# Performance work log

Hardware: AMD Instinct MI355X
Metric: run time of the kernel (lower is better)

The kernel has to match this reference:

```python
import jax, jax.numpy as jnp
import numpy as np

N = 1_000_000   # half-edges
C = 64          # in_channels == out_channels (out = empty_like(x))


def setup_inputs() -> dict:
    key = jax.random.key(0)
    k1, k2, k3, k4, k5, k6 = jax.random.split(key, 6)
    x = jax.random.normal(k1, (N, C), dtype=jnp.float32)
    next_idx = jax.random.randint(k2, (N,), 0, N, dtype=jnp.int32)
    twin_idx = jax.random.randint(k3, (N,), 0, N, dtype=jnp.int32)
    has_twin = jax.random.randint(k4, (N,), 0, 2, dtype=jnp.int32).astype(jnp.bool_)
    # nn.Linear(2C, C): weight [C, 2C], bias [C]; kaiming-uniform-ish init scale
    bound = 1.0 / np.sqrt(2 * C)
    W = jax.random.uniform(k5, (C, 2 * C), dtype=jnp.float32, minval=-bound, maxval=bound)
    b = jax.random.uniform(k6, (C,), dtype=jnp.float32, minval=-bound, maxval=bound)
    return {"x": x, "next_idx": next_idx, "twin_idx": twin_idx,
            "has_twin": has_twin, "W": W, "b": b}


def reference(x, next_idx, twin_idx, has_twin, W, b):
    # per-half-edge gather of next/twin vertex features (twin zero-filled if absent)
    next_f = x[next_idx]                                   # [N, C]
    twin_f = jnp.where(has_twin[:, None], x[twin_idx], 0.0)  # [N, C]
    neighbor = jnp.concatenate([next_f, twin_f], axis=-1)  # [N, 2C]
    out = neighbor @ W.T + b                               # [N, C]
    return jax.nn.relu(out)
```

## Files before the change

### kernel.cpp

```cpp
#include <hip/hip_runtime.h>
#include <hip/hip_bf16.h>
#include <stdint.h>

typedef __attribute__((ext_vector_type(4))) float f32x4;
typedef __attribute__((ext_vector_type(8))) __bf16 bf16x8;

#define NROWS 1000000

__device__ __forceinline__ bf16x8 cvt8(f32x4 a, f32x4 b) {
    bf16x8 r;
    r[0] = (__bf16)a[0]; r[1] = (__bf16)a[1];
    r[2] = (__bf16)a[2]; r[3] = (__bf16)a[3];
    r[4] = (__bf16)b[0]; r[5] = (__bf16)b[1];
    r[6] = (__bf16)b[2]; r[7] = (__bf16)b[3];
    return r;
}

__global__ void heconv_mfma(const float* __restrict__ x,
                            const int* __restrict__ nidx,
                            const int* __restrict__ tidx,
                            const int* __restrict__ ht,
                            const float* __restrict__ W,
                            const float* __restrict__ bias,
                            float* __restrict__ out)
{
    const int lane = threadIdx.x & 63;
    const int wave = threadIdx.x >> 6;
    const int lrow = lane & 15;
    const int lkg  = lane >> 4;

    bf16x8 wfrag[4][4];
#pragma unroll
    for (int ct = 0; ct < 4; ++ct) {
        const float* wrow = W + (ct * 16 + lrow) * 128 + lkg * 8;
#pragma unroll
        for (int ks = 0; ks < 4; ++ks) {
            f32x4 w0 = *(const f32x4*)(wrow + ks * 32);
            f32x4 w1 = *(const f32x4*)(wrow + ks * 32 + 4);
            wfrag[ct][ks] = cvt8(w0, w1);
        }
    }
    f32x4 bfrag[4];
#pragma unroll
    for (int ct = 0; ct < 4; ++ct)
        bfrag[ct] = *(const f32x4*)(bias + ct * 16 + lkg * 4);

    const int nGroups = NROWS / 16;
    const int gstride = gridDim.x * 4;
    const int g0 = blockIdx.x * 4 + wave;

    int ni = 0, ti = 0, htv = 0;
    if (g0 < nGroups) {
        int r = g0 * 16 + lrow;
        ni = nidx[r]; ti = tidx[r]; htv = ht[r];
    }

    const f32x4 z = {0.f, 0.f, 0.f, 0.f};

    for (int g = g0; g < nGroups; g += gstride) {
        const float* pn = x + (size_t)ni * 64 + lkg * 8;
        f32x4 n0 = *(const f32x4*)(pn);
        f32x4 n1 = *(const f32x4*)(pn + 4);
        f32x4 n2 = *(const f32x4*)(pn + 32);
        f32x4 n3 = *(const f32x4*)(pn + 36);

        f32x4 t0 = z, t1 = z, t2 = z, t3 = z;
        if (htv) {
            const float* pt = x + (size_t)ti * 64 + lkg * 8;
            t0 = *(const f32x4*)(pt);
            t1 = *(const f32x4*)(pt + 4);
            t2 = *(const f32x4*)(pt + 32);
            t3 = *(const f32x4*)(pt + 36);
        }

        const int gn = g + gstride;
        int ni2 = 0, ti2 = 0, htv2 = 0;
        if (gn < nGroups) {
            int r = gn * 16 + lrow;
            ni2 = nidx[r]; ti2 = tidx[r]; htv2 = ht[r];
        }

        bf16x8 xf[4] = { cvt8(n0, n1), cvt8(n2, n3),
                         cvt8(t0, t1), cvt8(t2, t3) };
        const int r = g * 16 + lrow;
#pragma unroll
        for (int ct = 0; ct < 4; ++ct) {
            f32x4 acc = bfrag[ct];
#pragma unroll
            for (int ks = 0; ks < 4; ++ks)
                acc = __builtin_amdgcn_mfma_f32_16x16x32_bf16(wfrag[ct][ks], xf[ks], acc, 0, 0, 0);
            f32x4 o;
            o[0] = fmaxf(acc[0], 0.f);
            o[1] = fmaxf(acc[1], 0.f);
            o[2] = fmaxf(acc[2], 0.f);
            o[3] = fmaxf(acc[3], 0.f);
            *(f32x4*)(out + (size_t)r * 64 + ct * 16 + lkg * 4) = o;
        }

        ni = ni2; ti = ti2; htv = htv2;
    }
}

extern "C" void kernel_launch(void* const* d_in, const int* in_sizes, int n_in,
                              void* d_out, int out_size, void* d_ws, size_t ws_size,
                              hipStream_t stream) {
    const float* x    = (const float*)d_in[0];
    const int*   ni   = (const int*)d_in[1];
    const int*   ti   = (const int*)d_in[2];
    const int*   ht   = (const int*)d_in[3];
    const float* W    = (const float*)d_in[4];
    const float* bias = (const float*)d_in[5];
    float*       out  = (float*)d_out;

    heconv_mfma<<<2048, 256, 0, stream>>>(x, ni, ti, ht, W, bias, out);
}
```

Baseline: 156.8 us.

## Software-pipeline row gathers one iteration ahead and stage W fragments in LDS

The gathered x rows for the next group are now loaded before the current group's MFMAs run, and indices are prefetched two groups ahead, so gather latency overlaps compute. Weight fragments move from registers into shared memory, read per MFMA, and launch bounds of 256 threads with 4 blocks per CU are added. The aim is lower register pressure and higher occupancy plus latency hiding, at the cost of LDS reads in the inner loop and more live registers for the prefetched rows. The first-group load now runs without a bounds check.

Result: slower. 219.8 us (+40.2%).

```diff
diff --git a/kernel.cpp b/kernel.cpp
--- a/kernel.cpp
+++ b/kernel.cpp
@@ -16,79 +16,109 @@
     return r;
 }
 
-__global__ void heconv_mfma(const float* __restrict__ x,
-                            const int* __restrict__ nidx,
-                            const int* __restrict__ tidx,
-                            const int* __restrict__ ht,
-                            const float* __restrict__ W,
-                            const float* __restrict__ bias,
-                            float* __restrict__ out)
+__global__ __launch_bounds__(256, 4)
+void heconv_mfma(const float* __restrict__ x,
+                 const int* __restrict__ nidx,
+                 const int* __restrict__ tidx,
+                 const int* __restrict__ ht,
+                 const float* __restrict__ W,
+                 const float* __restrict__ bias,
+                 float* __restrict__ out)
 {
-    const int lane = threadIdx.x & 63;
-    const int wave = threadIdx.x >> 6;
+    __shared__ bf16x8 wlds[4][4][64];
+
+    const int tid  = threadIdx.x;
+    const int lane = tid & 63;
+    const int wave = tid >> 6;
     const int lrow = lane & 15;
     const int lkg  = lane >> 4;
 
-    bf16x8 wfrag[4][4];
-#pragma unroll
-    for (int ct = 0; ct < 4; ++ct) {
-        const float* wrow = W + (ct * 16 + lrow) * 128 + lkg * 8;
-#pragma unroll
-        for (int ks = 0; ks < 4; ++ks) {
-            f32x4 w0 = *(const f32x4*)(wrow + ks * 32);
-            f32x4 w1 = *(const f32x4*)(wrow + ks * 32 + 4);
-            wfrag[ct][ks] = cvt8(w0, w1);
-        }
+    for (int e = tid; e < 1024; e += 256) {
+        const int l  = e & 63;
+        const int ks = (e >> 6) & 3;
+        const int ct = e >> 8;
+        const float* wr = W + (ct * 16 + (l & 15)) * 128 + ks * 32 + (l >> 4) * 8;
+        f32x4 w0 = *(const f32x4*)(wr);
+        f32x4 w1 = *(const f32x4*)(wr + 4);
+        wlds[ct][ks][l] = cvt8(w0, w1);
     }
     f32x4 bfrag[4];
 #pragma unroll
     for (int ct = 0; ct < 4; ++ct)
         bfrag[ct] = *(const f32x4*)(bias + ct * 16 + lkg * 4);
+    __syncthreads();
 
     const int nGroups = NROWS / 16;
     const int gstride = gridDim.x * 4;
     const int g0 = blockIdx.x * 4 + wave;
 
-    int ni = 0, ti = 0, htv = 0;
-    if (g0 < nGroups) {
-        int r = g0 * 16 + lrow;
-        ni = nidx[r]; ti = tidx[r]; htv = ht[r];
-    }
-
     const f32x4 z = {0.f, 0.f, 0.f, 0.f};
 
-    for (int g = g0; g < nGroups; g += gstride) {
+    f32x4 n0, n1, n2, n3, t0, t1, t2, t3;
+    {
+        const int r = g0 * 16 + lrow;
+        const int ni = nidx[r];
+        const int tv = tidx[r];
+        const int hv = ht[r];
         const float* pn = x + (size_t)ni * 64 + lkg * 8;
-        f32x4 n0 = *(const f32x4*)(pn);
-        f32x4 n1 = *(const f32x4*)(pn + 4);
-        f32x4 n2 = *(const f32x4*)(pn + 32);
-        f32x4 n3 = *(const f32x4*)(pn + 36);
-
-        f32x4 t0 = z, t1 = z, t2 = z, t3 = z;
-        if (htv) {
-            const float* pt = x + (size_t)ti * 64 + lkg * 8;
+        n0 = *(const f32x4*)(pn);
+        n1 = *(const f32x4*)(pn + 4);
+        n2 = *(const f32x4*)(pn + 32);
+        n3 = *(const f32x4*)(pn + 36);
+        t0 = z; t1 = z; t2 = z; t3 = z;
+        if (hv) {
+            const float* pt = x + (size_t)tv * 64 + lkg * 8;
             t0 = *(const f32x4*)(pt);
             t1 = *(const f32x4*)(pt + 4);
             t2 = *(const f32x4*)(pt + 32);
             t3 = *(const f32x4*)(pt + 36);
         }
+    }
+    int niN = 0, tiN = 0, hvN = 0;
+    if (g0 + gstride < nGroups) {
+        const int r = (g0 + gstride) * 16 + lrow;
+        niN = nidx[r]; tiN = tidx[r]; hvN = ht[r];
+    }
 
-        const int gn = g + gstride;
-        int ni2 = 0, ti2 = 0, htv2 = 0;
-        if (gn < nGroups) {
-            int r = gn * 16 + lrow;
-            ni2 = nidx[r]; ti2 = tidx[r]; htv2 = ht[r];
+    for (int g = g0; g < nGroups; g += gstride) {
+        const int gN = g + gstride;
+
+        bf16x8 xf0 = cvt8(n0, n1);
+        bf16x8 xf1 = cvt8(n2, n3);
+        bf16x8 xf2 = cvt8(t0, t1);
+        bf16x8 xf3 = cvt8(t2, t3);
+
+        if (gN < nGroups) {
+            const float* pn = x + (size_t)niN * 64 + lkg * 8;
+            n0 = *(const f32x4*)(pn);
+            n1 = *(const f32x4*)(pn + 4);
+            n2 = *(const f32x4*)(pn + 32);
+            n3 = *(const f32x4*)(pn + 36);
+            t0 = z; t1 = z; t2 = z; t3 = z;
+            if (hvN) {
+                const float* pt = x + (size_t)tiN * 64 + lkg * 8;
+                t0 = *(const f32x4*)(pt);
+                t1 = *(const f32x4*)(pt + 4);
+                t2 = *(const f32x4*)(pt + 32);
+                t3 = *(const f32x4*)(pt + 36);
+            }
         }
 
-        bf16x8 xf[4] = { cvt8(n0, n1), cvt8(n2, n3),
-                         cvt8(t0, t1), cvt8(t2, t3) };
+        int ni2 = 0, ti2 = 0, hv2 = 0;
+        const int g2 = g + 2 * gstride;
+        if (g2 < nGroups) {
+            const int r = g2 * 16 + lrow;
+            ni2 = nidx[r]; ti2 = tidx[r]; hv2 = ht[r];
+        }
+
         const int r = g * 16 + lrow;
+        bf16x8 xf[4] = { xf0, xf1, xf2, xf3 };
 #pragma unroll
         for (int ct = 0; ct < 4; ++ct) {
             f32x4 acc = bfrag[ct];
 #pragma unroll
             for (int ks = 0; ks < 4; ++ks)
-                acc = __builtin_amdgcn_mfma_f32_16x16x32_bf16(wfrag[ct][ks], xf[ks], acc, 0, 0, 0);
+                acc = __builtin_amdgcn_mfma_f32_16x16x32_bf16(wlds[ct][ks][lane], xf[ks], acc, 0, 0, 0);
             f32x4 o;
             o[0] = fmaxf(acc[0], 0.f);
             o[1] = fmaxf(acc[1], 0.f);
@@ -97,7 +127,7 @@
             *(f32x4*)(out + (size_t)r * 64 + ct * 16 + lkg * 4) = o;
         }
 
-        ni = ni2; ti = ti2; htv = htv2;
+        niN = ni2; tiN = ti2; hvN = hv2;
     }
 }
 
```

## Double-buffer gathered features in registers and shrink grid to persistent waves

Applied to the files above, without the earlier changes.

Restructures the grid-stride loop into two interleaved stages (A/B). Each stage keeps its gathered x rows in registers one iteration ahead, with indices prefetched two iterations ahead. This lets the scattered loads overlap with the MFMA work. The grid is reduced to 512 blocks with launch bounds and sched_barriers to fix the instruction order. The trade-off is fewer resident waves, and therefore less latency hiding from occupancy, plus higher register pressure.

New measurement: 137.3 us, median of 2. 12.4% less time.

```diff
diff --git a/kernel.cpp b/kernel.cpp
--- a/kernel.cpp
+++ b/kernel.cpp
@@ -16,13 +16,14 @@
     return r;
 }
 
-__global__ void heconv_mfma(const float* __restrict__ x,
-                            const int* __restrict__ nidx,
-                            const int* __restrict__ tidx,
-                            const int* __restrict__ ht,
-                            const float* __restrict__ W,
-                            const float* __restrict__ bias,
-                            float* __restrict__ out)
+__global__ __launch_bounds__(256, 2)
+void heconv_mfma(const float* __restrict__ x,
+                 const int* __restrict__ nidx,
+                 const int* __restrict__ tidx,
+                 const int* __restrict__ ht,
+                 const float* __restrict__ W,
+                 const float* __restrict__ bias,
+                 float* __restrict__ out)
 {
     const int lane = threadIdx.x & 63;
     const int wave = threadIdx.x >> 6;
@@ -46,58 +47,162 @@
         bfrag[ct] = *(const f32x4*)(bias + ct * 16 + lkg * 4);
 
     const int nGroups = NROWS / 16;
-    const int gstride = gridDim.x * 4;
+    const int S  = gridDim.x * 4;
     const int g0 = blockIdx.x * 4 + wave;
 
-    int ni = 0, ti = 0, htv = 0;
-    if (g0 < nGroups) {
-        int r = g0 * 16 + lrow;
-        ni = nidx[r]; ti = tidx[r]; htv = ht[r];
-    }
-
     const f32x4 z = {0.f, 0.f, 0.f, 0.f};
 
-    for (int g = g0; g < nGroups; g += gstride) {
+    f32x4 pAn0, pAn1, pAn2, pAn3, pAt0, pAt1, pAt2, pAt3;
+    f32x4 pBn0, pBn1, pBn2, pBn3, pBt0, pBt1, pBt2, pBt3;
+
+    {
+        const int r = g0 * 16 + lrow;
+        const int ni = nidx[r], tv = tidx[r], hv = ht[r];
         const float* pn = x + (size_t)ni * 64 + lkg * 8;
-        f32x4 n0 = *(const f32x4*)(pn);
-        f32x4 n1 = *(const f32x4*)(pn + 4);
-        f32x4 n2 = *(const f32x4*)(pn + 32);
-        f32x4 n3 = *(const f32x4*)(pn + 36);
-
-        f32x4 t0 = z, t1 = z, t2 = z, t3 = z;
-        if (htv) {
-            const float* pt = x + (size_t)ti * 64 + lkg * 8;
-            t0 = *(const f32x4*)(pt);
-            t1 = *(const f32x4*)(pt + 4);
-            t2 = *(const f32x4*)(pt + 32);
-            t3 = *(const f32x4*)(pt + 36);
-        }
-
-        const int gn = g + gstride;
-        int ni2 = 0, ti2 = 0, htv2 = 0;
-        if (gn < nGroups) {
-            int r = gn * 16 + lrow;
-            ni2 = nidx[r]; ti2 = tidx[r]; htv2 = ht[r];
-        }
-
-        bf16x8 xf[4] = { cvt8(n0, n1), cvt8(n2, n3),
-                         cvt8(t0, t1), cvt8(t2, t3) };
-        const int r = g * 16 + lrow;
-#pragma unroll
-        for (int ct = 0; ct < 4; ++ct) {
-            f32x4 acc = bfrag[ct];
-#pragma unroll
-            for (int ks = 0; ks < 4; ++ks)
-                acc = __builtin_amdgcn_mfma_f32_16x16x32_bf16(wfrag[ct][ks], xf[ks], acc, 0, 0, 0);
-            f32x4 o;
-            o[0] = fmaxf(acc[0], 0.f);
-            o[1] = fmaxf(acc[1], 0.f);
-            o[2] = fmaxf(acc[2], 0.f);
-            o[3] = fmaxf(acc[3], 0.f);
-            *(f32x4*)(out + (size_t)r * 64 + ct * 16 + lkg * 4) = o;
-        }
-
-        ni = ni2; ti = ti2; htv = htv2;
+        pAn0 = *(const f32x4*)(pn);
+        pAn1 = *(const f32x4*)(pn + 4);
+        pAn2 = *(const f32x4*)(pn + 32);
+        pAn3 = *(const f32x4*)(pn + 36);
+        pAt0 = z; pAt1 = z; pAt2 = z; pAt3 = z;
+        if (hv) {
+            const float* pt = x + (size_t)tv * 64 + lkg * 8;
+            pAt0 = *(const f32x4*)(pt);
+            pAt1 = *(const f32x4*)(pt + 4);
+            pAt2 = *(const f32x4*)(pt + 32);
+            pAt3 = *(const f32x4*)(pt + 36);
+        }
+    }
+    pBn0 = z; pBn1 = z; pBn2 = z; pBn3 = z;
+    pBt0 = z; pBt1 = z; pBt2 = z; pBt3 = z;
+    if (g0 + S < nGroups) {
+        const int r = (g0 + S) * 16 + lrow;
+        const int ni = nidx[r], tv = tidx[r], hv = ht[r];
+        const float* pn = x + (size_t)ni * 64 + lkg * 8;
+        pBn0 = *(const f32x4*)(pn);
+        pBn1 = *(const f32x4*)(pn + 4);
+        pBn2 = *(const f32x4*)(pn + 32);
+        pBn3 = *(const f32x4*)(pn + 36);
+        if (hv) {
+            const float* pt = x + (size_t)tv * 64 + lkg * 8;
+            pBt0 = *(const f32x4*)(pt);
+            pBt1 = *(const f32x4*)(pt + 4);
+            pBt2 = *(const f32x4*)(pt + 32);
+            pBt3 = *(const f32x4*)(pt + 36);
+        }
+    }
+
+    int aNi = 0, aTi = 0, aHv = 0, bNi = 0, bTi = 0, bHv = 0;
+    if (g0 + 2 * S < nGroups) {
+        const int r = (g0 + 2 * S) * 16 + lrow;
+        aNi = nidx[r]; aTi = tidx[r]; aHv = ht[r];
+    }
+    if (g0 + 3 * S < nGroups) {
+        const int r = (g0 + 3 * S) * 16 + lrow;
+        bNi = nidx[r]; bTi = tidx[r]; bHv = ht[r];
+    }
+
+    for (int g = g0; g < nGroups; g += 2 * S) {
+        {
+            bf16x8 xf0 = cvt8(pAn0, pAn1);
+            bf16x8 xf1 = cvt8(pAn2, pAn3);
+            bf16x8 xf2 = cvt8(pAt0, pAt1);
+            bf16x8 xf3 = cvt8(pAt2, pAt3);
+
+            __builtin_amdgcn_sched_barrier(0);
+
+            if (g + 2 * S < nGroups) {
+                const float* pn = x + (size_t)aNi * 64 + lkg * 8;
+                pAn0 = *(const f32x4*)(pn);
+                pAn1 = *(const f32x4*)(pn + 4);
+                pAn2 = *(const f32x4*)(pn + 32);
+                pAn3 = *(const f32x4*)(pn + 36);
+                pAt0 = z; pAt1 = z; pAt2 = z; pAt3 = z;
+                if (aHv) {
+                    const float* pt = x + (size_t)aTi * 64 + lkg * 8;
+                    pAt0 = *(const f32x4*)(pt);
+                    pAt1 = *(const f32x4*)(pt + 4);
+                    pAt2 = *(const f32x4*)(pt + 32);
+                    pAt3 = *(const f32x4*)(pt + 36);
+                }
+            }
+
+            __builtin_amdgcn_sched_barrier(0);
+
+            aNi = 0; aTi = 0; aHv = 0;
+            if (g + 4 * S < nGroups) {
+                const int r = (g + 4 * S) * 16 + lrow;
+                aNi = nidx[r]; aTi = tidx[r]; aHv = ht[r];
+            }
+
+            const int r = g * 16 + lrow;
+            bf16x8 xf[4] = { xf0, xf1, xf2, xf3 };
+#pragma unroll
+            for (int ct = 0; ct < 4; ++ct) {
+                f32x4 acc = bfrag[ct];
+#pragma unroll
+                for (int ks = 0; ks < 4; ++ks)
+                    acc = __builtin_amdgcn_mfma_f32_16x16x32_bf16(wfrag[ct][ks], xf[ks], acc, 0, 0, 0);
+                f32x4 o;
+                o[0] = fmaxf(acc[0], 0.f);
+                o[1] = fmaxf(acc[1], 0.f);
+                o[2] = fmaxf(acc[2], 0.f);
+                o[3] = fmaxf(acc[3], 0.f);
+                *(f32x4*)(out + (size_t)r * 64 + ct * 16 + lkg * 4) = o;
+            }
+
+            __builtin_amdgcn_sched_barrier(0);
+        }
+
+        if (g + S < nGroups) {
+            bf16x8 xf0 = cvt8(pBn0, pBn1);
+            bf16x8 xf1 = cvt8(pBn2, pBn3);
+            bf16x8 xf2 = cvt8(pBt0, pBt1);
+            bf16x8 xf3 = cvt8(pBt2, pBt3);
+
+            __builtin_amdgcn_sched_barrier(0);
+
+            if (g + 3 * S < nGroups) {
+                const float* pn = x + (size_t)bNi * 64 + lkg * 8;
+                pBn0 = *(const f32x4*)(pn);
+                pBn1 = *(const f32x4*)(pn + 4);
+                pBn2 = *(const f32x4*)(pn + 32);
+                pBn3 = *(const f32x4*)(pn + 36);
+                pBt0 = z; pBt1 = z; pBt2 = z; pBt3 = z;
+                if (bHv) {
+                    const float* pt = x + (size_t)bTi * 64 + lkg * 8;
+                    pBt0 = *(const f32x4*)(pt);
+                    pBt1 = *(const f32x4*)(pt + 4);
+                    pBt2 = *(const f32x4*)(pt + 32);
+                    pBt3 = *(const f32x4*)(pt + 36);
+                }
+            }
+
+            __builtin_amdgcn_sched_barrier(0);
+
+            bNi = 0; bTi = 0; bHv = 0;
+            if (g + 5 * S < nGroups) {
+                const int r = (g + 5 * S) * 16 + lrow;
+                bNi = nidx[r]; bTi = tidx[r]; bHv = ht[r];
+            }
+
+            const int r = (g + S) * 16 + lrow;
+            bf16x8 xf[4] = { xf0, xf1, xf2, xf3 };
+#pragma unroll
+            for (int ct = 0; ct < 4; ++ct) {
+                f32x4 acc = bfrag[ct];
+#pragma unroll
+                for (int ks = 0; ks < 4; ++ks)
+                    acc = __builtin_amdgcn_mfma_f32_16x16x32_bf16(wfrag[ct][ks], xf[ks], acc, 0, 0, 0);
+                f32x4 o;
+                o[0] = fmaxf(acc[0], 0.f);
+                o[1] = fmaxf(acc[1], 0.f);
+                o[2] = fmaxf(acc[2], 0.f);
+                o[3] = fmaxf(acc[3], 0.f);
+                *(f32x4*)(out + (size_t)r * 64 + ct * 16 + lkg * 4) = o;
+            }
+
+            __builtin_amdgcn_sched_barrier(0);
+        }
     }
 }
 
@@ -112,5 +217,5 @@
     const float* bias = (const float*)d_in[5];
     float*       out  = (float*)d_out;
 
-    heconv_mfma<<<2048, 256, 0, stream>>>(x, ni, ti, ht, W, bias, out);
+    heconv_mfma<<<512, 256, 0, stream>>>(x, ni, ti, ht, W, bias, out);
 }
```
